# Kernel optimization log

Hardware: AMD Instinct MI355X
Metric: run time of the kernel (lower is better)

## Reference

```python
import jax, jax.numpy as jnp
import numpy as np

KEY_DIM = 1024
VALUE_DIM = 1024
NUM_HEADS = 16
ORIGIN_SHAPE = (8, 16, 16)  # T, H, W video-token grid
LOCAL_BLOCKS = 3
B = 1
S = int(np.prod(ORIGIN_SHAPE))  # 2048
DH = KEY_DIM // NUM_HEADS       # 64
DV = VALUE_DIM // NUM_HEADS


def make_layout():
    """Vectorized equivalent of SparseAttention.make_layout (causal=True)."""
    shape = np.array(ORIGIN_SHAPE, dtype=np.int64)
    cum = np.concatenate([np.flip(np.cumprod(np.flip(shape)))[1:], [1]]).astype(np.int64)
    idx = np.arange(S, dtype=np.int64)
    coords = (idx[None, :] // cum[:, None]) % shape[:, None]  # [ndim, S]
    diff = idx[:, None] - idx[None, :]
    layout = (diff >= 0) & (diff <= LOCAL_BLOCKS)  # causal local window
    for d in range(len(ORIGIN_SHAPE) - 1):  # causal axial strides along dims 0..ndim-2
        same = np.ones((S, S), dtype=bool)
        for e in range(len(ORIGIN_SHAPE)):
            if e != d:
                same &= coords[e][:, None] == coords[e][None, :]
        layout |= same & (coords[d][None, :] <= coords[d][:, None])
    return layout  # [S, S] bool


def setup_inputs() -> dict:
    key = jax.random.key(0)
    ks = jax.random.split(key, 11)
    sc = 0.02
    inp = {
        "query": jax.random.normal(ks[0], (B, S, KEY_DIM), jnp.float32),
        "key":   jax.random.normal(ks[1], (B, S, KEY_DIM), jnp.float32),
        "value": jax.random.normal(ks[2], (B, S, VALUE_DIM), jnp.float32),
        "wq": sc * jax.random.normal(ks[3], (KEY_DIM, KEY_DIM), jnp.float32),
        "bq": jnp.zeros((KEY_DIM,), jnp.float32),
        "wk": sc * jax.random.normal(ks[4], (KEY_DIM, KEY_DIM), jnp.float32),
        "bk": jnp.zeros((KEY_DIM,), jnp.float32),
        "wv": sc * jax.random.normal(ks[5], (VALUE_DIM, VALUE_DIM), jnp.float32),
        "bv": jnp.zeros((VALUE_DIM,), jnp.float32),
        "wo": sc * jax.random.normal(ks[6], (VALUE_DIM, KEY_DIM), jnp.float32),
        "bo": jnp.zeros((KEY_DIM,), jnp.float32),
        "layout": jnp.asarray(make_layout(), jnp.int32)[None, None],  # [1,1,S,S]
    }
    return inp


def reference(query, key, value, wq, bq, wk, bk, wv, bv, wo, bo, layout):
    def split(x, d):  # [B,S,H*d] -> [B,H,S,d]
        return x.reshape(B, S, NUM_HEADS, d).transpose(0, 2, 1, 3)
    q = split(query @ wq + bq, DH)
    k = split(key @ wk + bk, DH)
    v = split(value @ wv + bv, DV)
    logits = jnp.einsum('bhsd,bhtd->bhst', q, k) / jnp.sqrt(jnp.float32(DH))
    logits = jnp.where(layout > 0, logits, jnp.float32(-1e9))
    attn = jax.nn.softmax(logits, axis=-1)  # matches tf.sparse.softmax over layout support
    out = jnp.einsum('bhst,bhtd->bhsd', attn, v)
    out = out.transpose(0, 2, 1, 3).reshape(B, S, VALUE_DIM)
    return out @ wo + bo
```

## Files before the change

### kernel.cpp

```cpp
#include <hip/hip_runtime.h>
#include <hip/hip_bf16.h>
#include <cstdint>
#include <math.h>

#define SEQ    2048
#define DMODEL 1024
#define NHEAD  16
#define DHEAD  64
#define NZPAD  32

typedef __bf16 bf16;
typedef __bf16 bf16x4 __attribute__((ext_vector_type(4)));
typedef __bf16 bf16x8 __attribute__((ext_vector_type(8)));
typedef float  f32x4  __attribute__((ext_vector_type(4)));

typedef __attribute__((address_space(3))) uint32_t lds_u32;
typedef __attribute__((address_space(1))) const uint32_t global_u32;

__device__ __forceinline__ void async_load16(const void* g, void* l) {
    __builtin_amdgcn_global_load_lds((global_u32*)g, (lds_u32*)l, 16, 0, 0);
}

__device__ __forceinline__ int support_idx(int s, int c, int tt, int hh,
                                           int cnt) {
    const int jA = c * 256 + (s & 255);
    const int jB = (s & 0x700) + (c - tt) * 16 + (s & 15);
    const int jC = s - (cnt - 1 - c);
    return c < tt ? jA : (c < tt + hh ? jB : (c < cnt ? jC : s));
}

__global__ __launch_bounds__(256) void prep_tr_kernel(
    const float* __restrict__ w0, const float* __restrict__ w1,
    const float* __restrict__ w2, const float* __restrict__ w3,
    bf16* __restrict__ t0, bf16* __restrict__ t1,
    bf16* __restrict__ t2, bf16* __restrict__ t3) {
    __shared__ float tile[64][65];
    const int z = blockIdx.x >> 8, rem = blockIdx.x & 255;
    const float* w = (z == 0) ? w0 : (z == 1) ? w1 : (z == 2) ? w2 : w3;
    bf16* t        = (z == 0) ? t0 : (z == 1) ? t1 : (z == 2) ? t2 : t3;
    const int kb = (rem >> 4) * 64, nb = (rem & 15) * 64;
    const int c4 = threadIdx.x & 15, rg = threadIdx.x >> 4;
#pragma unroll
    for (int i = 0; i < 4; ++i) {
        const int row = rg * 4 + i;
        const float4 v = *(const float4*)&w[(size_t)(kb + row) * DMODEL + nb + c4 * 4];
        tile[row][c4 * 4 + 0] = v.x; tile[row][c4 * 4 + 1] = v.y;
        tile[row][c4 * 4 + 2] = v.z; tile[row][c4 * 4 + 3] = v.w;
    }
    __syncthreads();
#pragma unroll
    for (int i = 0; i < 4; ++i) {
        const int n = rg * 4 + i;
        bf16x4 o;
        o[0] = (bf16)tile[c4 * 4 + 0][n]; o[1] = (bf16)tile[c4 * 4 + 1][n];
        o[2] = (bf16)tile[c4 * 4 + 2][n]; o[3] = (bf16)tile[c4 * 4 + 3][n];
        *(bf16x4*)&t[(size_t)(nb + n) * DMODEL + kb + c4 * 4] = o;
    }
}

__global__ __launch_bounds__(256) void proj3_kernel(
    const float* __restrict__ qf, const float* __restrict__ kf, const float* __restrict__ vf,
    const bf16* __restrict__ wqT, const bf16* __restrict__ wkT, const bf16* __restrict__ wvT,
    const float* __restrict__ bq, const float* __restrict__ bk, const float* __restrict__ bv,
    bf16* __restrict__ qp, bf16* __restrict__ kp, bf16* __restrict__ vp) {
    constexpr int K = 1024, N = 1024, BK = 64, TM = 64, MI = 2;
    const int z = blockIdx.z;
    const float* A  = (z == 0) ? qf : (z == 1) ? kf : vf;
    const bf16* BT  = (z == 0) ? wqT : (z == 1) ? wkT : wvT;
    const float* bi = (z == 0) ? bq : (z == 1) ? bk : bv;
    bf16* C         = (z == 0) ? qp : (z == 1) ? kp : vp;

    __shared__ bf16 sA[2][TM * BK];
    __shared__ bf16 sB[2][128 * BK];
    const int tid = threadIdx.x;
    const int w = tid >> 6, lane = tid & 63;
    const int wm = w >> 1, wn = w & 1;
    const int lr = lane & 15, quad = lane >> 4;
    const int m0 = blockIdx.y * TM, n0 = blockIdx.x * 128;
    const int ar = tid >> 2, ak4 = tid & 3;

    f32x4 acc[MI][4] = {};
    float bia[4];
#pragma unroll
    for (int ni = 0; ni < 4; ++ni) bia[ni] = bi[n0 + wn * 64 + ni * 16 + lr];

    float4 av[4];
    auto issueA = [&](int kt) {
        const float4* src = (const float4*)(A + (size_t)(m0 + ar) * K + kt + ak4 * 16);
#pragma unroll
        for (int i = 0; i < 4; ++i) av[i] = src[i];
    };
    auto writeA = [&](int buf) {
        bf16x8 c0, c1;
        c0[0] = (bf16)av[0].x; c0[1] = (bf16)av[0].y; c0[2] = (bf16)av[0].z; c0[3] = (bf16)av[0].w;
        c0[4] = (bf16)av[1].x; c0[5] = (bf16)av[1].y; c0[6] = (bf16)av[1].z; c0[7] = (bf16)av[1].w;
        c1[0] = (bf16)av[2].x; c1[1] = (bf16)av[2].y; c1[2] = (bf16)av[2].z; c1[3] = (bf16)av[2].w;
        c1[4] = (bf16)av[3].x; c1[5] = (bf16)av[3].y; c1[6] = (bf16)av[3].z; c1[7] = (bf16)av[3].w;
        const int s0 = (ak4 * 2) ^ (ar & 7), s1 = (ak4 * 2 + 1) ^ (ar & 7);
        *(bf16x8*)&sA[buf][ar * BK + s0 * 8] = c0;
        *(bf16x8*)&sA[buf][ar * BK + s1 * 8] = c1;
    };
    auto gloadB = [&](int buf, int kt) {
#pragma unroll
        for (int kk = 0; kk < 4; ++kk) {
            const int cb = kk * 256 + w * 64;
            const int p = cb + lane;
            const int row = p >> 3, chl = p & 7;
            const int chg = chl ^ (row & 7);
            async_load16(BT + (size_t)(n0 + row) * K + kt + chg * 8,
                         (char*)&sB[buf][0] + cb * 16);
        }
    };

    issueA(0);
    gloadB(0, 0);
    writeA(0);
    asm volatile("s_waitcnt vmcnt(0) lgkmcnt(0)" ::: "memory");
    __builtin_amdgcn_s_barrier();
    __builtin_amdgcn_sched_barrier(0);

    int cur = 0;
    for (int kt = 0; kt < K; kt += BK) {
        const bool more = (kt + BK) < K;
        if (more) { issueA(kt + BK); gloadB(cur ^ 1, kt + BK); }
#pragma unroll
        for (int ks = 0; ks < 2; ++ks) {
            bf16x8 af[MI], bfr[4];
#pragma unroll
            for (int mi = 0; mi < MI; ++mi) {
                const int row = wm * (TM / 2) + mi * 16 + lr;
                af[mi] = *(const bf16x8*)
                    &sA[cur][row * BK + ((ks * 4 + quad) ^ (row & 7)) * 8];
            }
#pragma unroll
            for (int ni = 0; ni < 4; ++ni) {
                const int row = wn * 64 + ni * 16 + lr;
                bfr[ni] = *(const bf16x8*)
                    &sB[cur][row * BK + ((ks * 4 + quad) ^ (row & 7)) * 8];
            }
            __builtin_amdgcn_s_setprio(1);
#pragma unroll
            for (int mi = 0; mi < MI; ++mi)
#pragma unroll
                for (int ni = 0; ni < 4; ++ni)
                    acc[mi][ni] = __builtin_amdgcn_mfma_f32_16x16x32_bf16(
                        af[mi], bfr[ni], acc[mi][ni], 0, 0, 0);
            __builtin_amdgcn_s_setprio(0);
        }
        if (more) writeA(cur ^ 1);
        asm volatile("s_waitcnt vmcnt(0) lgkmcnt(0)" ::: "memory");
        __builtin_amdgcn_s_barrier();
        __builtin_amdgcn_sched_barrier(0);
        cur ^= 1;
    }

#pragma unroll
    for (int mi = 0; mi < MI; ++mi)
#pragma unroll
        for (int ni = 0; ni < 4; ++ni) {
            const int row = m0 + wm * (TM / 2) + mi * 16 + quad * 4;
            const int col = n0 + wn * 64 + ni * 16 + lr;
            const f32x4 vv = acc[mi][ni];
#pragma unroll
            for (int r = 0; r < 4; ++r)
                C[(size_t)(row + r) * N + col] = (bf16)(vv[r] + bia[ni]);
        }
}

__global__ __launch_bounds__(256) void gemm_final_kernel(
    const bf16* __restrict__ A, const bf16* __restrict__ BT,
    const float* __restrict__ bias, float* __restrict__ C) {
    constexpr int K = 1024, N = 1024, BK = 64, TM = 32, MI = 1;
    constexpr int ACH = TM * (BK / 8);
    constexpr int TCH = ACH + 128 * (BK / 8);
    __shared__ bf16 sA[2][TM * BK];
    __shared__ bf16 sB[2][128 * BK];
    const int tid = threadIdx.x;
    const int w = tid >> 6, lane = tid & 63;
    const int wm = w >> 1, wn = w & 1;
    const int lr = lane & 15, quad = lane >> 4;
    const int m0 = blockIdx.y * TM, n0 = blockIdx.x * 128;

    f32x4 acc[MI][4] = {};
    float bia[4];
#pragma unroll
    for (int ni = 0; ni < 4; ++ni) bia[ni] = bias[n0 + wn * 64 + ni * 16 + lr];

    auto stage = [&](int buf, int kt) {
#pragma unroll
        for (int kk = 0; kk < TCH / 256; ++kk) {
            const int cb = kk * 256 + w * 64;
            const int p = cb + lane;
            if (cb < ACH) {
                const int row = p >> 3, chl = p & 7;
                const int chg = chl ^ (row & 7);
                async_load16(A + (size_t)(m0 + row) * K + kt + chg * 8,
                             (char*)&sA[buf][0] + cb * 16);
            } else {
                const int p2 = p - ACH, row = p2 >> 3, chl = p2 & 7;
                const int chg = chl ^ (row & 7);
                async_load16(BT + (size_t)(n0 + row) * K + kt + chg * 8,
                             (char*)&sB[buf][0] + (cb - ACH) * 16);
            }
        }
    };

    stage(0, 0);
    asm volatile("s_waitcnt vmcnt(0)" ::: "memory");
    __builtin_amdgcn_s_barrier();
    __builtin_amdgcn_sched_barrier(0);

    int cur = 0;
    for (int kt = 0; kt < K; kt += BK) {
        if (kt + BK < K) stage(cur ^ 1, kt + BK);
#pragma unroll
        for (int ks = 0; ks < 2; ++ks) {
            bf16x8 af[MI], bfr[4];
#pragma unroll
            for (int mi = 0; mi < MI; ++mi) {
                const int row = wm * (TM / 2) + mi * 16 + lr;
                af[mi] = *(const bf16x8*)
                    &sA[cur][row * BK + ((ks * 4 + quad) ^ (row & 7)) * 8];
            }
#pragma unroll
            for (int ni = 0; ni < 4; ++ni) {
                const int row = wn * 64 + ni * 16 + lr;
                bfr[ni] = *(const bf16x8*)
                    &sB[cur][row * BK + ((ks * 4 + quad) ^ (row & 7)) * 8];
            }
            __builtin_amdgcn_s_setprio(1);
#pragma unroll
            for (int mi = 0; mi < MI; ++mi)
#pragma unroll
                for (int ni = 0; ni < 4; ++ni)
                    acc[mi][ni] = __builtin_amdgcn_mfma_f32_16x16x32_bf16(
                        af[mi], bfr[ni], acc[mi][ni], 0, 0, 0);
            __builtin_amdgcn_s_setprio(0);
        }
        asm volatile("s_waitcnt vmcnt(0)" ::: "memory");
        __builtin_amdgcn_s_barrier();
        __builtin_amdgcn_sched_barrier(0);
        cur ^= 1;
    }

#pragma unroll
    for (int mi = 0; mi < MI; ++mi)
#pragma unroll
        for (int ni = 0; ni < 4; ++ni) {
            const int row = m0 + wm * (TM / 2) + mi * 16 + quad * 4;
            const int col = n0 + wn * 64 + ni * 16 + lr;
            const f32x4 vv = acc[mi][ni];
#pragma unroll
            for (int r = 0; r < 4; ++r)
                C[(size_t)(row + r) * N + col] = vv[r] + bia[ni];
        }
}

__global__ __launch_bounds__(256) void attn_kernel(
    const bf16* __restrict__ qp, const bf16* __restrict__ kp, const bf16* __restrict__ vp,
    bf16* __restrict__ ao) {
    const int wv = threadIdx.x >> 6, lane = threadIdx.x & 63;
    constexpr int NB = NHEAD * SEQ / 4;
    const int bid = (blockIdx.x & 7) * (NB >> 3) + (blockIdx.x >> 3);
    const int p = bid * 4 + wv;
    const int s = __builtin_amdgcn_readfirstlane(p & (SEQ - 1));
    const int h = __builtin_amdgcn_readfirstlane(p >> 11);
    const int hbase = h * DHEAD;
    const int hoff = hbase + lane;

    const int tt = (s >> 8) & 7, hh = (s >> 4) & 15;
    const int win = (s < 3) ? s : 3;
    const int cnt = tt + hh + win + 1;

    int t[NZPAD];
#pragma unroll
    for (int c = 0; c < NZPAD; ++c) t[c] = support_idx(s, c, tt, hh, cnt);

    const int c_lane = lane & 31;
    const int fo = (lane >> 5) << 5;
    const int myT = support_idx(s, c_lane, tt, hh, cnt);

    const bf16x8* qrow = (const bf16x8*)(qp + (size_t)s * DMODEL + hbase + fo);
    const bf16x8* krow = (const bf16x8*)(kp + (size_t)myT * DMODEL + hbase + fo);
    bf16x8 qc[4], kc[4];
#pragma unroll
    for (int j = 0; j < 4; ++j) { qc[j] = qrow[j]; kc[j] = krow[j]; }

    float vvv[NZPAD];
#pragma unroll
    for (int c = 0; c < NZPAD; ++c)
        vvv[c] = (float)vp[(size_t)t[c] * DMODEL + hoff];

    float dot = 0.f;
#pragma unroll
    for (int j = 0; j < 4; ++j)
#pragma unroll
        for (int e = 0; e < 8; ++e)
            dot = fmaf((float)qc[j][e], (float)kc[j][e], dot);
    dot += __shfl_xor(dot, 32);

    const float logit = (c_lane < cnt) ? dot * 0.125f : -1e30f;
    float m = logit;
    m = fmaxf(m, __shfl_xor(m, 1)); m = fmaxf(m, __shfl_xor(m, 2));
    m = fmaxf(m, __shfl_xor(m, 4)); m = fmaxf(m, __shfl_xor(m, 8));
    m = fmaxf(m, __shfl_xor(m, 16));
    const float e = __expf(logit - m);
    float ssum = e;
    ssum += __shfl_xor(ssum, 1); ssum += __shfl_xor(ssum, 2);
    ssum += __shfl_xor(ssum, 4); ssum += __shfl_xor(ssum, 8);
    ssum += __shfl_xor(ssum, 16);
    const float prob = e / ssum;

    float acc = 0.f;
#pragma unroll
    for (int c = 0; c < NZPAD; ++c) {
        const float pc = __uint_as_float(
            __builtin_amdgcn_readlane(__float_as_uint(prob), c));
        acc = fmaf(pc, vvv[c], acc);
    }
    ao[(size_t)s * DMODEL + hoff] = (bf16)acc;
}

extern "C" void kernel_launch(void* const* d_in, const int* in_sizes, int n_in,
                              void* d_out, int out_size, void* d_ws, size_t ws_size,
                              hipStream_t stream) {
    const float* query = (const float*)d_in[0];
    const float* key   = (const float*)d_in[1];
    const float* value = (const float*)d_in[2];
    const float* wq = (const float*)d_in[3];
    const float* bq = (const float*)d_in[4];
    const float* wk = (const float*)d_in[5];
    const float* bk = (const float*)d_in[6];
    const float* wv = (const float*)d_in[7];
    const float* bv = (const float*)d_in[8];
    const float* wo = (const float*)d_in[9];
    const float* bo = (const float*)d_in[10];
    float* out = (float*)d_out;

    char* ws = (char*)d_ws;
    auto alloc = [&](size_t bytes) {
        char* p = ws;
        ws += (bytes + 255) & ~(size_t)255;
        return p;
    };
    bf16* wqT = (bf16*)alloc((size_t)DMODEL * DMODEL * 2);
    bf16* wkT = (bf16*)alloc((size_t)DMODEL * DMODEL * 2);
    bf16* wvT = (bf16*)alloc((size_t)DMODEL * DMODEL * 2);
    bf16* woT = (bf16*)alloc((size_t)DMODEL * DMODEL * 2);
    bf16* qp  = (bf16*)alloc((size_t)SEQ * DMODEL * 2);
    bf16* kp  = (bf16*)alloc((size_t)SEQ * DMODEL * 2);
    bf16* vp  = (bf16*)alloc((size_t)SEQ * DMODEL * 2);
    bf16* ao  = (bf16*)alloc((size_t)SEQ * DMODEL * 2);

    prep_tr_kernel<<<dim3(1024), 256, 0, stream>>>(
        wq, wk, wv, wo, wqT, wkT, wvT, woT);
    proj3_kernel<<<dim3(8, 32, 3), 256, 0, stream>>>(
        query, key, value, wqT, wkT, wvT, bq, bk, bv, qp, kp, vp);
    attn_kernel<<<dim3(NHEAD * SEQ / 4), 256, 0, stream>>>(qp, kp, vp, ao);
    gemm_final_kernel<<<dim3(8, 64), 256, 0, stream>>>(ao, woT, bo, out);
}
```

Baseline: 172.3 us.

## Pre-cast activations to bf16, triple-stage async GEMM pipelines, remap blocks

The prep kernel now also casts query/key/value to bf16 and uses 32x32 transpose tiles. That lets proj3 load A through async global-to-LDS copies instead of register conversion. Both GEMMs move to a two-ahead prefetch with partial vmcnt waits and an XCD-aware block remapping. gemm_final changes its warp layout, and the attention kernel adds setprio around its FMA loops. The cost is an extra 12 MB round trip through workspace for the casted activations.

Result: faster. 159.4 us (median of 2 runs) (-7.5%).

```diff
diff --git a/kernel.cpp b/kernel.cpp
--- a/kernel.cpp
+++ b/kernel.cpp
@@ -10,7 +10,6 @@
 #define NZPAD  32
 
 typedef __bf16 bf16;
-typedef __bf16 bf16x4 __attribute__((ext_vector_type(4)));
 typedef __bf16 bf16x8 __attribute__((ext_vector_type(8)));
 typedef float  f32x4  __attribute__((ext_vector_type(4)));
 
@@ -29,43 +28,63 @@
     return c < tt ? jA : (c < tt + hh ? jB : (c < cnt ? jC : s));
 }
 
-__global__ __launch_bounds__(256) void prep_tr_kernel(
+#define CAST_BLOCKS 3072
+#define TR_BLOCKS   4096
+
+__global__ __launch_bounds__(256) void prep_kernel(
+    const float* __restrict__ q, const float* __restrict__ k, const float* __restrict__ v,
+    bf16* __restrict__ qx, bf16* __restrict__ kx, bf16* __restrict__ vx,
     const float* __restrict__ w0, const float* __restrict__ w1,
     const float* __restrict__ w2, const float* __restrict__ w3,
     bf16* __restrict__ t0, bf16* __restrict__ t1,
     bf16* __restrict__ t2, bf16* __restrict__ t3) {
-    __shared__ float tile[64][65];
-    const int z = blockIdx.x >> 8, rem = blockIdx.x & 255;
-    const float* w = (z == 0) ? w0 : (z == 1) ? w1 : (z == 2) ? w2 : w3;
-    bf16* t        = (z == 0) ? t0 : (z == 1) ? t1 : (z == 2) ? t2 : t3;
-    const int kb = (rem >> 4) * 64, nb = (rem & 15) * 64;
-    const int c4 = threadIdx.x & 15, rg = threadIdx.x >> 4;
-#pragma unroll
-    for (int i = 0; i < 4; ++i) {
-        const int row = rg * 4 + i;
-        const float4 v = *(const float4*)&w[(size_t)(kb + row) * DMODEL + nb + c4 * 4];
-        tile[row][c4 * 4 + 0] = v.x; tile[row][c4 * 4 + 1] = v.y;
-        tile[row][c4 * 4 + 2] = v.z; tile[row][c4 * 4 + 3] = v.w;
+    __shared__ float tile[32][33];
+    const int bid = blockIdx.x;
+    if (bid < CAST_BLOCKS) {
+        const int z = bid >> 10;
+        const float* src = (z == 0) ? q : (z == 1) ? k : v;
+        bf16* dst        = (z == 0) ? qx : (z == 1) ? kx : vx;
+        const int i = (bid & 1023) * 256 + threadIdx.x;
+        const float4* s4 = (const float4*)src;
+        float4 a = s4[i * 2 + 0];
+        float4 b = s4[i * 2 + 1];
+        bf16x8 o;
+        o[0] = (bf16)a.x; o[1] = (bf16)a.y; o[2] = (bf16)a.z; o[3] = (bf16)a.w;
+        o[4] = (bf16)b.x; o[5] = (bf16)b.y; o[6] = (bf16)b.z; o[7] = (bf16)b.w;
+        ((bf16x8*)dst)[i] = o;
+    } else {
+        const int b = bid - CAST_BLOCKS;
+        const int z = b >> 10, rem = b & 1023;
+        const float* w = (z == 0) ? w0 : (z == 1) ? w1 : (z == 2) ? w2 : w3;
+        bf16* t        = (z == 0) ? t0 : (z == 1) ? t1 : (z == 2) ? t2 : t3;
+        const int tx = threadIdx.x & 31, ty = threadIdx.x >> 5;
+        const int kbase = (rem >> 5) * 32, nbase = (rem & 31) * 32;
+#pragma unroll
+        for (int i = 0; i < 4; ++i)
+            tile[ty + 8 * i][tx] = w[(size_t)(kbase + ty + 8 * i) * DMODEL + nbase + tx];
+        __syncthreads();
+#pragma unroll
+        for (int i = 0; i < 4; ++i)
+            t[(size_t)(nbase + ty + 8 * i) * DMODEL + kbase + tx] = (bf16)tile[tx][ty + 8 * i];
     }
-    __syncthreads();
-#pragma unroll
-    for (int i = 0; i < 4; ++i) {
-        const int n = rg * 4 + i;
-        bf16x4 o;
-        o[0] = (bf16)tile[c4 * 4 + 0][n]; o[1] = (bf16)tile[c4 * 4 + 1][n];
-        o[2] = (bf16)tile[c4 * 4 + 2][n]; o[3] = (bf16)tile[c4 * 4 + 3][n];
-        *(bf16x4*)&t[(size_t)(nb + n) * DMODEL + kb + c4 * 4] = o;
-    }
 }
 
 __global__ __launch_bounds__(256) void proj3_kernel(
-    const float* __restrict__ qf, const float* __restrict__ kf, const float* __restrict__ vf,
+    const bf16* __restrict__ qx, const bf16* __restrict__ kx, const bf16* __restrict__ vx,
     const bf16* __restrict__ wqT, const bf16* __restrict__ wkT, const bf16* __restrict__ wvT,
     const float* __restrict__ bq, const float* __restrict__ bk, const float* __restrict__ bv,
     bf16* __restrict__ qp, bf16* __restrict__ kp, bf16* __restrict__ vp) {
     constexpr int K = 1024, N = 1024, BK = 64, TM = 64, MI = 2;
-    const int z = blockIdx.z;
-    const float* A  = (z == 0) ? qf : (z == 1) ? kf : vf;
+    constexpr int ACH = TM * (BK / 8);
+    constexpr int TCH = ACH + 128 * (BK / 8);
+
+    const int orig = blockIdx.x;
+    const int flat = (orig & 7) * 96 + (orig >> 3);
+    const int z = flat >> 8;
+    const int rem = flat & 255;
+    const int m0 = (rem >> 3) * TM, n0 = (rem & 7) * 128;
+
+    const bf16* A   = (z == 0) ? qx : (z == 1) ? kx : vx;
     const bf16* BT  = (z == 0) ? wqT : (z == 1) ? wkT : wvT;
     const float* bi = (z == 0) ? bq : (z == 1) ? bk : bv;
     bf16* C         = (z == 0) ? qp : (z == 1) ? kp : vp;
@@ -76,53 +95,42 @@
     const int w = tid >> 6, lane = tid & 63;
     const int wm = w >> 1, wn = w & 1;
     const int lr = lane & 15, quad = lane >> 4;
-    const int m0 = blockIdx.y * TM, n0 = blockIdx.x * 128;
-    const int ar = tid >> 2, ak4 = tid & 3;
 
     f32x4 acc[MI][4] = {};
     float bia[4];
 #pragma unroll
     for (int ni = 0; ni < 4; ++ni) bia[ni] = bi[n0 + wn * 64 + ni * 16 + lr];
 
-    float4 av[4];
-    auto issueA = [&](int kt) {
-        const float4* src = (const float4*)(A + (size_t)(m0 + ar) * K + kt + ak4 * 16);
-#pragma unroll
-        for (int i = 0; i < 4; ++i) av[i] = src[i];
+    auto stage = [&](int buf, int kt) {
+#pragma unroll
+        for (int kk = 0; kk < TCH / 256; ++kk) {
+            const int cb = kk * 256 + w * 64;
+            const int p  = cb + lane;
+            if (cb < ACH) {
+                const int row = p >> 3, chl = p & 7;
+                const int chg = chl ^ (row & 7);
+                async_load16(A + (size_t)(m0 + row) * K + kt + chg * 8,
+                             (char*)&sA[buf][0] + cb * 16);
+            } else {
+                const int p2 = p - ACH, row = p2 >> 3, chl = p2 & 7;
+                const int chg = chl ^ (row & 7);
+                async_load16(BT + (size_t)(n0 + row) * K + kt + chg * 8,
+                             (char*)&sB[buf][0] + (cb - ACH) * 16);
+            }
+        }
     };
-    auto writeA = [&](int buf) {
-        bf16x8 c0, c1;
-        c0[0] = (bf16)av[0].x; c0[1] = (bf16)av[0].y; c0[2] = (bf16)av[0].z; c0[3] = (bf16)av[0].w;
-        c0[4] = (bf16)av[1].x; c0[5] = (bf16)av[1].y; c0[6] = (bf16)av[1].z; c0[7] = (bf16)av[1].w;
-        c1[0] = (bf16)av[2].x; c1[1] = (bf16)av[2].y; c1[2] = (bf16)av[2].z; c1[3] = (bf16)av[2].w;
-        c1[4] = (bf16)av[3].x; c1[5] = (bf16)av[3].y; c1[6] = (bf16)av[3].z; c1[7] = (bf16)av[3].w;
-        const int s0 = (ak4 * 2) ^ (ar & 7), s1 = (ak4 * 2 + 1) ^ (ar & 7);
-        *(bf16x8*)&sA[buf][ar * BK + s0 * 8] = c0;
-        *(bf16x8*)&sA[buf][ar * BK + s1 * 8] = c1;
-    };
-    auto gloadB = [&](int buf, int kt) {
-#pragma unroll
-        for (int kk = 0; kk < 4; ++kk) {
-            const int cb = kk * 256 + w * 64;
-            const int p = cb + lane;
-            const int row = p >> 3, chl = p & 7;
-            const int chg = chl ^ (row & 7);
-            async_load16(BT + (size_t)(n0 + row) * K + kt + chg * 8,
-                         (char*)&sB[buf][0] + cb * 16);
-        }
-    };
-
-    issueA(0);
-    gloadB(0, 0);
-    writeA(0);
-    asm volatile("s_waitcnt vmcnt(0) lgkmcnt(0)" ::: "memory");
-    __builtin_amdgcn_s_barrier();
-    __builtin_amdgcn_sched_barrier(0);
-
+
+    stage(0, 0);
+    stage(1, BK);
     int cur = 0;
     for (int kt = 0; kt < K; kt += BK) {
-        const bool more = (kt + BK) < K;
-        if (more) { issueA(kt + BK); gloadB(cur ^ 1, kt + BK); }
+        if (kt + BK < K) {
+            asm volatile("s_waitcnt vmcnt(6)" ::: "memory");
+        } else {
+            asm volatile("s_waitcnt vmcnt(0)" ::: "memory");
+        }
+        __builtin_amdgcn_s_barrier();
+        __builtin_amdgcn_sched_barrier(0);
 #pragma unroll
         for (int ks = 0; ks < 2; ++ks) {
             bf16x8 af[MI], bfr[4];
@@ -147,10 +155,9 @@
                         af[mi], bfr[ni], acc[mi][ni], 0, 0, 0);
             __builtin_amdgcn_s_setprio(0);
         }
-        if (more) writeA(cur ^ 1);
-        asm volatile("s_waitcnt vmcnt(0) lgkmcnt(0)" ::: "memory");
         __builtin_amdgcn_s_barrier();
         __builtin_amdgcn_sched_barrier(0);
+        if (kt + 2 * BK < K) stage(cur, kt + 2 * BK);
         cur ^= 1;
     }
 
@@ -170,21 +177,24 @@
 __global__ __launch_bounds__(256) void gemm_final_kernel(
     const bf16* __restrict__ A, const bf16* __restrict__ BT,
     const float* __restrict__ bias, float* __restrict__ C) {
-    constexpr int K = 1024, N = 1024, BK = 64, TM = 32, MI = 1;
+    constexpr int K = 1024, N = 1024, BK = 64, TM = 32, MI = 2;
     constexpr int ACH = TM * (BK / 8);
     constexpr int TCH = ACH + 128 * (BK / 8);
+
+    const int orig = blockIdx.x;
+    const int flat = (orig & 7) * 64 + (orig >> 3);
+    const int m0 = (flat >> 3) * TM, n0 = (flat & 7) * 128;
+
     __shared__ bf16 sA[2][TM * BK];
     __shared__ bf16 sB[2][128 * BK];
     const int tid = threadIdx.x;
     const int w = tid >> 6, lane = tid & 63;
-    const int wm = w >> 1, wn = w & 1;
     const int lr = lane & 15, quad = lane >> 4;
-    const int m0 = blockIdx.y * TM, n0 = blockIdx.x * 128;
-
-    f32x4 acc[MI][4] = {};
-    float bia[4];
-#pragma unroll
-    for (int ni = 0; ni < 4; ++ni) bia[ni] = bias[n0 + wn * 64 + ni * 16 + lr];
+
+    f32x4 acc[MI][2] = {};
+    float bia[2];
+#pragma unroll
+    for (int ni = 0; ni < 2; ++ni) bia[ni] = bias[n0 + w * 32 + ni * 16 + lr];
 
     auto stage = [&](int buf, int kt) {
 #pragma unroll
@@ -206,25 +216,28 @@
     };
 
     stage(0, 0);
-    asm volatile("s_waitcnt vmcnt(0)" ::: "memory");
-    __builtin_amdgcn_s_barrier();
-    __builtin_amdgcn_sched_barrier(0);
-
+    stage(1, BK);
     int cur = 0;
     for (int kt = 0; kt < K; kt += BK) {
-        if (kt + BK < K) stage(cur ^ 1, kt + BK);
+        if (kt + BK < K) {
+            asm volatile("s_waitcnt vmcnt(5)" ::: "memory");
+        } else {
+            asm volatile("s_waitcnt vmcnt(0)" ::: "memory");
+        }
+        __builtin_amdgcn_s_barrier();
+        __builtin_amdgcn_sched_barrier(0);
 #pragma unroll
         for (int ks = 0; ks < 2; ++ks) {
-            bf16x8 af[MI], bfr[4];
+            bf16x8 af[MI], bfr[2];
 #pragma unroll
             for (int mi = 0; mi < MI; ++mi) {
-                const int row = wm * (TM / 2) + mi * 16 + lr;
+                const int row = mi * 16 + lr;
                 af[mi] = *(const bf16x8*)
                     &sA[cur][row * BK + ((ks * 4 + quad) ^ (row & 7)) * 8];
             }
 #pragma unroll
-            for (int ni = 0; ni < 4; ++ni) {
-                const int row = wn * 64 + ni * 16 + lr;
+            for (int ni = 0; ni < 2; ++ni) {
+                const int row = w * 32 + ni * 16 + lr;
                 bfr[ni] = *(const bf16x8*)
                     &sB[cur][row * BK + ((ks * 4 + quad) ^ (row & 7)) * 8];
             }
@@ -232,23 +245,23 @@
 #pragma unroll
             for (int mi = 0; mi < MI; ++mi)
 #pragma unroll
-                for (int ni = 0; ni < 4; ++ni)
+                for (int ni = 0; ni < 2; ++ni)
                     acc[mi][ni] = __builtin_amdgcn_mfma_f32_16x16x32_bf16(
                         af[mi], bfr[ni], acc[mi][ni], 0, 0, 0);
             __builtin_amdgcn_s_setprio(0);
         }
-        asm volatile("s_waitcnt vmcnt(0)" ::: "memory");
         __builtin_amdgcn_s_barrier();
         __builtin_amdgcn_sched_barrier(0);
+        if (kt + 2 * BK < K) stage(cur, kt + 2 * BK);
         cur ^= 1;
     }
 
 #pragma unroll
     for (int mi = 0; mi < MI; ++mi)
 #pragma unroll
-        for (int ni = 0; ni < 4; ++ni) {
-            const int row = m0 + wm * (TM / 2) + mi * 16 + quad * 4;
-            const int col = n0 + wn * 64 + ni * 16 + lr;
+        for (int ni = 0; ni < 2; ++ni) {
+            const int row = m0 + mi * 16 + quad * 4;
+            const int col = n0 + w * 32 + ni * 16 + lr;
             const f32x4 vv = acc[mi][ni];
 #pragma unroll
             for (int r = 0; r < 4; ++r)
@@ -292,11 +305,13 @@
         vvv[c] = (float)vp[(size_t)t[c] * DMODEL + hoff];
 
     float dot = 0.f;
+    __builtin_amdgcn_s_setprio(1);
 #pragma unroll
     for (int j = 0; j < 4; ++j)
 #pragma unroll
         for (int e = 0; e < 8; ++e)
             dot = fmaf((float)qc[j][e], (float)kc[j][e], dot);
+    __builtin_amdgcn_s_setprio(0);
     dot += __shfl_xor(dot, 32);
 
     const float logit = (c_lane < cnt) ? dot * 0.125f : -1e30f;
@@ -312,12 +327,14 @@
     const float prob = e / ssum;
 
     float acc = 0.f;
+    __builtin_amdgcn_s_setprio(1);
 #pragma unroll
     for (int c = 0; c < NZPAD; ++c) {
         const float pc = __uint_as_float(
             __builtin_amdgcn_readlane(__float_as_uint(prob), c));
         acc = fmaf(pc, vvv[c], acc);
     }
+    __builtin_amdgcn_s_setprio(0);
     ao[(size_t)s * DMODEL + hoff] = (bf16)acc;
 }
 
@@ -343,6 +360,9 @@
         ws += (bytes + 255) & ~(size_t)255;
         return p;
     };
+    bf16* qx  = (bf16*)alloc((size_t)SEQ * DMODEL * 2);
+    bf16* kx  = (bf16*)alloc((size_t)SEQ * DMODEL * 2);
+    bf16* vx  = (bf16*)alloc((size_t)SEQ * DMODEL * 2);
     bf16* wqT = (bf16*)alloc((size_t)DMODEL * DMODEL * 2);
     bf16* wkT = (bf16*)alloc((size_t)DMODEL * DMODEL * 2);
     bf16* wvT = (bf16*)alloc((size_t)DMODEL * DMODEL * 2);
@@ -352,10 +372,11 @@
     bf16* vp  = (bf16*)alloc((size_t)SEQ * DMODEL * 2);
     bf16* ao  = (bf16*)alloc((size_t)SEQ * DMODEL * 2);
 
-    prep_tr_kernel<<<dim3(1024), 256, 0, stream>>>(
+    prep_kernel<<<dim3(CAST_BLOCKS + TR_BLOCKS), 256, 0, stream>>>(
+        query, key, value, qx, kx, vx,
         wq, wk, wv, wo, wqT, wkT, wvT, woT);
-    proj3_kernel<<<dim3(8, 32, 3), 256, 0, stream>>>(
-        query, key, value, wqT, wkT, wvT, bq, bk, bv, qp, kp, vp);
+    proj3_kernel<<<dim3(768), 256, 0, stream>>>(
+        qx, kx, vx, wqT, wkT, wvT, bq, bk, bv, qp, kp, vp);
     attn_kernel<<<dim3(NHEAD * SEQ / 4), 256, 0, stream>>>(qp, kp, vp, ao);
-    gemm_final_kernel<<<dim3(8, 64), 256, 0, stream>>>(ao, woT, bo, out);
-}
+    gemm_final_kernel<<<dim3(512), 256, 0, stream>>>(ao, woT, bo, out);
+}
```
